# Kernel optimization log

Measured on AMD Instinct MI355X. Metric: run time of the kernel, lower is better.

The kernel has to match this reference:

```python
import jax, jax.numpy as jnp
import numpy as np

M, K, N = 32, 8192, 28672

def setup_inputs() -> dict:
    key = jax.random.key(0)
    k1, k2, k3 = jax.random.split(key, 3)
    act = jax.random.normal(k1, (M, K), dtype=jnp.float16)
    # int8 quantized weight, stored as int8 (spec lists int32 for harness compat)
    weight = jax.random.randint(k2, (K, N), -127, 128, dtype=jnp.int8)
    # per-output-channel dequant scale, small positive values typical of fp8/int8 quant
    scale = (jax.random.uniform(k3, (1, N), dtype=jnp.float32) * 0.01 + 1e-4).astype(jnp.float16)
    return {"act": act, "weight": weight, "scale": scale}

def reference(act, weight, scale):
    # grouped_gemm with single group: out[m,n] = (sum_k act[m,k] * w[k,n]) * scale[n]
    # int8 weight is dequantized inline; accumulate in fp32, emit fp16 like the kernel.
    acc = jnp.einsum("mk,kn->mn", act.astype(jnp.float16), weight.astype(jnp.float16),
                     preferred_element_type=jnp.float32)
    out = acc * scale.astype(jnp.float32)
    return out.astype(jnp.float16)
```

## Files before the change

kernel.cpp:

```cpp
#include <hip/hip_runtime.h>
#include <hip/hip_bf16.h>

#define MM 32
#define KK 8192
#define NN 28672

typedef _Float16 half8   __attribute__((ext_vector_type(8)));
typedef __fp16   fp16x2  __attribute__((ext_vector_type(2)));
typedef float    floatx4 __attribute__((ext_vector_type(4)));
typedef int      intx4   __attribute__((ext_vector_type(4)));

__global__ __launch_bounds__(256) void act_cvt_kernel(
    const float* __restrict__ act, __fp16* __restrict__ act16)
{
    int i = (blockIdx.x * 256 + threadIdx.x) * 4;
    floatx4 v = *(const floatx4*)(act + i);
    fp16x2 lo = __builtin_amdgcn_cvt_pkrtz(v[0], v[1]);
    fp16x2 hi = __builtin_amdgcn_cvt_pkrtz(v[2], v[3]);
    __fp16* o = act16 + i;
    *(fp16x2*)(o)     = lo;
    *(fp16x2*)(o + 2) = hi;
}

#define BN 64
#define BK 128
#define LDSTRIDE 136

template <int KSPLIT>
__global__ __launch_bounds__(256) void gemm_staged_kernel(
    const __fp16*   __restrict__ act16,
    const int*      __restrict__ weight,
    float*          __restrict__ ws)
{
    __shared__ __fp16 tileB[BN * LDSTRIDE];

    const int t    = threadIdx.x;
    const int lane = t & 63;
    const int wave = t >> 6;
    const int col  = lane & 15;
    const int quad = lane >> 4;

    const int nblock = blockIdx.x * BN;
    const int kc     = blockIdx.y * (KK / KSPLIT);
    const int stages = (KK / KSPLIT) / BK;

    const int seg = t & 15;
    const int kg  = t >> 4;
    const int n0s = seg * 4;
    const int k0s = kg * 8;

    floatx4 acc0 = {0.f, 0.f, 0.f, 0.f};
    floatx4 acc1 = {0.f, 0.f, 0.f, 0.f};

    const int* wbase = weight + (size_t)(kc + k0s) * NN + nblock + n0s;
    const __fp16* abase = act16 + (size_t)col * KK + kc + quad * 8;

    for (int s = 0; s < stages; ++s) {
        intx4 w[8];
#pragma unroll
        for (int i = 0; i < 8; ++i)
            w[i] = *(const intx4*)(wbase + (size_t)(s * BK + i) * NN);

#pragma unroll
        for (int j = 0; j < 4; ++j) {
            fp16x2 p0 = __builtin_amdgcn_cvt_pkrtz((float)w[0][j], (float)w[1][j]);
            fp16x2 p1 = __builtin_amdgcn_cvt_pkrtz((float)w[2][j], (float)w[3][j]);
            fp16x2 p2 = __builtin_amdgcn_cvt_pkrtz((float)w[4][j], (float)w[5][j]);
            fp16x2 p3 = __builtin_amdgcn_cvt_pkrtz((float)w[6][j], (float)w[7][j]);
            __fp16* dst = tileB + (n0s + j) * LDSTRIDE + k0s;
            *(fp16x2*)(dst)     = p0;
            *(fp16x2*)(dst + 2) = p1;
            *(fp16x2*)(dst + 4) = p2;
            *(fp16x2*)(dst + 6) = p3;
        }
        __syncthreads();

        const __fp16* brow = tileB + (wave * 16 + col) * LDSTRIDE;
        const __fp16* ak   = abase + s * BK;
#pragma unroll
        for (int kb = 0; kb < BK / 32; ++kb) {
            half8 b  = *(const half8*)(brow + kb * 32 + quad * 8);
            half8 a0 = *(const half8*)(ak + kb * 32);
            half8 a1 = *(const half8*)(ak + kb * 32 + (size_t)16 * KK);
            acc0 = __builtin_amdgcn_mfma_f32_16x16x32_f16(a0, b, acc0, 0, 0, 0);
            acc1 = __builtin_amdgcn_mfma_f32_16x16x32_f16(a1, b, acc1, 0, 0, 0);
        }
        __syncthreads();
    }

    float* wsb = ws + (size_t)blockIdx.y * MM * NN + nblock + wave * 16 + col;
#pragma unroll
    for (int r = 0; r < 4; ++r) {
        int m0 = quad * 4 + r;
        wsb[(size_t)m0 * NN]        = acc0[r];
        wsb[(size_t)(m0 + 16) * NN] = acc1[r];
    }
}

template <int KSPLIT>
__global__ __launch_bounds__(256) void finalize_kernel(
    const float* __restrict__ ws,
    const float* __restrict__ scale,
    float*       __restrict__ out)
{
    const int n = blockIdx.x * 256 + threadIdx.x;
    const int m = blockIdx.y;
    float sum = 0.f;
#pragma unroll
    for (int c = 0; c < KSPLIT; ++c)
        sum += ws[(size_t)c * MM * NN + (size_t)m * NN + n];
    out[(size_t)m * NN + n] = sum * scale[n];
}

__global__ __launch_bounds__(256) void gemm_direct_kernel(
    const float* __restrict__ act,
    const int*   __restrict__ weight,
    const float* __restrict__ scale,
    float*       __restrict__ out)
{
    const int lane = threadIdx.x & 63;
    const int wave = threadIdx.x >> 6;
    const int col  = lane & 15;
    const int quad = lane >> 4;
    const int n0 = blockIdx.x * 64 + wave * 16 + col;

    floatx4 acc0 = {0.f, 0.f, 0.f, 0.f};
    floatx4 acc1 = {0.f, 0.f, 0.f, 0.f};
    const float* ap0 = act + (size_t)col * KK + quad * 8;
    const float* ap1 = ap0 + (size_t)16 * KK;
    const int* wp = weight + (size_t)(quad * 8) * NN + n0;

    for (int s = 0; s < KK / 32; ++s) {
        floatx4 a0lo = *(const floatx4*)(ap0);
        floatx4 a0hi = *(const floatx4*)(ap0 + 4);
        floatx4 a1lo = *(const floatx4*)(ap1);
        floatx4 a1hi = *(const floatx4*)(ap1 + 4);
        half8 a0, a1, b;
#pragma unroll
        for (int j = 0; j < 4; ++j) {
            a0[j] = (_Float16)a0lo[j]; a0[j + 4] = (_Float16)a0hi[j];
            a1[j] = (_Float16)a1lo[j]; a1[j + 4] = (_Float16)a1hi[j];
        }
#pragma unroll
        for (int j = 0; j < 8; ++j)
            b[j] = (_Float16)wp[(size_t)j * NN];
        acc0 = __builtin_amdgcn_mfma_f32_16x16x32_f16(a0, b, acc0, 0, 0, 0);
        acc1 = __builtin_amdgcn_mfma_f32_16x16x32_f16(a1, b, acc1, 0, 0, 0);
        ap0 += 32; ap1 += 32; wp += (size_t)32 * NN;
    }
    float sc = scale[n0];
#pragma unroll
    for (int r = 0; r < 4; ++r) {
        int m0 = quad * 4 + r;
        out[(size_t)m0 * NN + n0]        = acc0[r] * sc;
        out[(size_t)(m0 + 16) * NN + n0] = acc1[r] * sc;
    }
}

extern "C" void kernel_launch(void* const* d_in, const int* in_sizes, int n_in,
                              void* d_out, int out_size, void* d_ws, size_t ws_size,
                              hipStream_t stream)
{
    const float* act    = (const float*)d_in[0];
    const int*   weight = (const int*)d_in[1];
    const float* scale  = (const float*)d_in[2];
    float*       out    = (float*)d_out;

    constexpr int KSPLIT = 4;
    const size_t partials_bytes = (size_t)KSPLIT * MM * NN * sizeof(float);
    const size_t act16_off      = partials_bytes;
    const size_t need           = act16_off + (size_t)MM * KK * sizeof(__fp16);

    if (ws_size >= need) {
        float*   ws_part = (float*)d_ws;
        __fp16*  act16   = (__fp16*)((char*)d_ws + act16_off);

        act_cvt_kernel<<<MM * KK / (256 * 4), 256, 0, stream>>>(act, act16);

        dim3 grid(NN / BN, KSPLIT);
        gemm_staged_kernel<KSPLIT><<<grid, 256, 0, stream>>>(act16, weight, ws_part);

        dim3 fgrid(NN / 256, MM);
        finalize_kernel<KSPLIT><<<fgrid, 256, 0, stream>>>(ws_part, scale, out);
    } else {
        gemm_direct_kernel<<<NN / 64, 256, 0, stream>>>(act, weight, scale, out);
    }
}
```

Before: 1.200 ms.

## Replace LDS-staged weight tile with register double-buffered direct streaming

Removes the shared-memory staging of the dequantized weight tile and its two barriers per stage. Each lane now loads its own eight weight elements straight from global memory into registers, using a two-buffer software pipeline so the next step's loads are in flight while the current step converts and runs MFMA. The cost is scalar 4-byte loads with a 32-row stride instead of 16-byte vector loads, which may reduce coalescing efficiency. The launch bounds also ask for 6 blocks per CU.

New measurement: 1.263 ms. 5.3% more time.

```diff
diff --git a/kernel.cpp b/kernel.cpp
--- a/kernel.cpp
+++ b/kernel.cpp
@@ -8,7 +8,6 @@
 typedef _Float16 half8   __attribute__((ext_vector_type(8)));
 typedef __fp16   fp16x2  __attribute__((ext_vector_type(2)));
 typedef float    floatx4 __attribute__((ext_vector_type(4)));
-typedef int      intx4   __attribute__((ext_vector_type(4)));
 
 __global__ __launch_bounds__(256) void act_cvt_kernel(
     const float* __restrict__ act, __fp16* __restrict__ act16)
@@ -22,73 +21,69 @@
     *(fp16x2*)(o + 2) = hi;
 }
 
-#define BN 64
-#define BK 128
-#define LDSTRIDE 136
-
 template <int KSPLIT>
-__global__ __launch_bounds__(256) void gemm_staged_kernel(
+__global__ __launch_bounds__(256, 6) void gemm_stream_kernel(
     const __fp16*   __restrict__ act16,
     const int*      __restrict__ weight,
     float*          __restrict__ ws)
 {
-    __shared__ __fp16 tileB[BN * LDSTRIDE];
-
-    const int t    = threadIdx.x;
-    const int lane = t & 63;
-    const int wave = t >> 6;
+    const int lane = threadIdx.x & 63;
+    const int wave = threadIdx.x >> 6;
     const int col  = lane & 15;
     const int quad = lane >> 4;
 
-    const int nblock = blockIdx.x * BN;
-    const int kc     = blockIdx.y * (KK / KSPLIT);
-    const int stages = (KK / KSPLIT) / BK;
+    const int n0 = blockIdx.x * 64 + wave * 16 + col;
+    const int kc = blockIdx.y * (KK / KSPLIT);
+    constexpr int NSTEP = (KK / KSPLIT) / 32;
 
-    const int seg = t & 15;
-    const int kg  = t >> 4;
-    const int n0s = seg * 4;
-    const int k0s = kg * 8;
+    const int*    wp  = weight + (size_t)(kc + quad * 8) * NN + n0;
+    const __fp16* ap0 = act16 + (size_t)col * KK + kc + quad * 8;
+    const __fp16* ap1 = ap0 + (size_t)16 * KK;
 
     floatx4 acc0 = {0.f, 0.f, 0.f, 0.f};
     floatx4 acc1 = {0.f, 0.f, 0.f, 0.f};
 
-    const int* wbase = weight + (size_t)(kc + k0s) * NN + nblock + n0s;
-    const __fp16* abase = act16 + (size_t)col * KK + kc + quad * 8;
+    int   wA[8], wB[8];
+    half8 aA0, aA1, aB0, aB1;
 
-    for (int s = 0; s < stages; ++s) {
-        intx4 w[8];
+    auto load_step = [&](int (&w)[8], half8& a0, half8& a1) {
 #pragma unroll
-        for (int i = 0; i < 8; ++i)
-            w[i] = *(const intx4*)(wbase + (size_t)(s * BK + i) * NN);
+        for (int j = 0; j < 8; ++j)
+            w[j] = wp[(size_t)j * NN];
+        a0 = *(const half8*)ap0;
+        a1 = *(const half8*)ap1;
+        wp  += (size_t)32 * NN;
+        ap0 += 32;
+        ap1 += 32;
+    };
 
+    auto compute_step = [&](const int (&w)[8], const half8 a0, const half8 a1) {
+        half8 b;
 #pragma unroll
         for (int j = 0; j < 4; ++j) {
-            fp16x2 p0 = __builtin_amdgcn_cvt_pkrtz((float)w[0][j], (float)w[1][j]);
-            fp16x2 p1 = __builtin_amdgcn_cvt_pkrtz((float)w[2][j], (float)w[3][j]);
-            fp16x2 p2 = __builtin_amdgcn_cvt_pkrtz((float)w[4][j], (float)w[5][j]);
-            fp16x2 p3 = __builtin_amdgcn_cvt_pkrtz((float)w[6][j], (float)w[7][j]);
-            __fp16* dst = tileB + (n0s + j) * LDSTRIDE + k0s;
-            *(fp16x2*)(dst)     = p0;
-            *(fp16x2*)(dst + 2) = p1;
-            *(fp16x2*)(dst + 4) = p2;
-            *(fp16x2*)(dst + 6) = p3;
+            fp16x2 p = __builtin_amdgcn_cvt_pkrtz((float)w[2 * j],
+                                                  (float)w[2 * j + 1]);
+            b[2 * j]     = p[0];
+            b[2 * j + 1] = p[1];
         }
-        __syncthreads();
+        acc0 = __builtin_amdgcn_mfma_f32_16x16x32_f16(a0, b, acc0, 0, 0, 0);
+        acc1 = __builtin_amdgcn_mfma_f32_16x16x32_f16(a1, b, acc1, 0, 0, 0);
+    };
 
-        const __fp16* brow = tileB + (wave * 16 + col) * LDSTRIDE;
-        const __fp16* ak   = abase + s * BK;
-#pragma unroll
-        for (int kb = 0; kb < BK / 32; ++kb) {
-            half8 b  = *(const half8*)(brow + kb * 32 + quad * 8);
-            half8 a0 = *(const half8*)(ak + kb * 32);
-            half8 a1 = *(const half8*)(ak + kb * 32 + (size_t)16 * KK);
-            acc0 = __builtin_amdgcn_mfma_f32_16x16x32_f16(a0, b, acc0, 0, 0, 0);
-            acc1 = __builtin_amdgcn_mfma_f32_16x16x32_f16(a1, b, acc1, 0, 0, 0);
-        }
-        __syncthreads();
+    load_step(wA, aA0, aA1);
+#pragma unroll 1
+    for (int s = 0; s < NSTEP / 2 - 1; ++s) {
+        load_step(wB, aB0, aB1);
+        compute_step(wA, aA0, aA1);
+        load_step(wA, aA0, aA1);
+        compute_step(wB, aB0, aB1);
     }
+    load_step(wB, aB0, aB1);
+    compute_step(wA, aA0, aA1);
+    compute_step(wB, aB0, aB1);
 
-    float* wsb = ws + (size_t)blockIdx.y * MM * NN + nblock + wave * 16 + col;
+    float* wsb = ws + (size_t)blockIdx.y * MM * NN + blockIdx.x * 64
+               + wave * 16 + col;
 #pragma unroll
     for (int r = 0; r < 4; ++r) {
         int m0 = quad * 4 + r;
@@ -177,8 +172,8 @@
 
         act_cvt_kernel<<<MM * KK / (256 * 4), 256, 0, stream>>>(act, act16);
 
-        dim3 grid(NN / BN, KSPLIT);
-        gemm_staged_kernel<KSPLIT><<<grid, 256, 0, stream>>>(act16, weight, ws_part);
+        dim3 grid(NN / 64, KSPLIT);
+        gemm_stream_kernel<KSPLIT><<<grid, 256, 0, stream>>>(act16, weight, ws_part);
 
         dim3 fgrid(NN / 256, MM);
         finalize_kernel<KSPLIT><<<fgrid, 256, 0, stream>>>(ws_part, scale, out);
```
